# Optimization experiments

Hardware: AMD Instinct MI355X
Metric: run time of the kernel (lower is better)

The kernel has to match this reference:

```python
import jax, jax.numpy as jnp
import numpy as np

K = 16            # neighbors
RATIO = 0.25      # sampling ratio
BN_EPS = 1e-5


def setup_inputs() -> dict:
    key = jax.random.key(0)
    k1, k2, k3 = jax.random.split(key, 3)
    B, N, Cin, Cout = 8, 8192, 64, 128
    x = jax.random.normal(k1, (B, N, Cin), dtype=jnp.float32)
    p1 = jax.random.uniform(k2, (B, N, 3), dtype=jnp.float32)
    W = jax.random.normal(k3, (Cout, Cin), dtype=jnp.float32) * 0.05  # Conv1d(k=1, bias=False)
    gamma = jnp.ones((Cout,), dtype=jnp.float32)   # BatchNorm1d weight
    beta = jnp.zeros((Cout,), dtype=jnp.float32)   # BatchNorm1d bias
    return {"x": x, "p1": p1, "W": W, "gamma": gamma, "beta": beta}


def furthest_point_sample(p, M):
    """Greedy FPS. p: (B,N,3) -> (B,M) int32 indices. Starts at index 0 (CUDA impl convention)."""
    B, N, _ = p.shape
    first = jnp.zeros((B,), dtype=jnp.int32)
    mind = jnp.full((B, N), 1e10, dtype=p.dtype)

    def step(carry, _):
        mind, last = carry
        lp = jnp.take_along_axis(p, last[:, None, None].astype(jnp.int32), axis=1)  # (B,1,3)
        d = jnp.sum((p - lp) ** 2, axis=-1)          # (B,N)
        mind = jnp.minimum(mind, d)
        nxt = jnp.argmax(mind, axis=1).astype(jnp.int32)
        return (mind, nxt), nxt

    (_, _), rest = jax.lax.scan(step, (mind, first), None, length=M - 1)  # rest: (M-1,B)
    idx = jnp.concatenate([first[None, :], rest], axis=0)  # (M,B)
    return idx.T  # (B,M)


def reference(x, p1, W, gamma, beta):
    B, N, Cin = x.shape
    M = int(N * RATIO)

    # --- FPS sampling + gather coords ---
    fps_idx = furthest_point_sample(p1, M)                      # (B,M)
    p2 = jnp.take_along_axis(p1, fps_idx[:, :, None], axis=1)   # (B,M,3)

    # --- brute-force kNN of p1 around each p2 query ---
    d2 = (jnp.sum(p2 ** 2, -1)[:, :, None]
          - 2.0 * jnp.einsum('bmd,bnd->bmn', p2, p1)
          + jnp.sum(p1 ** 2, -1)[:, None, :])                   # (B,M,N)
    _, nbr = jax.lax.top_k(-d2, K)                              # (B,M,K) indices into N

    # --- shared MLP: 1x1 conv (no bias) + BatchNorm1d (training-mode stats) + ReLU ---
    h = jnp.einsum('bnc,oc->bno', x, W)                         # (B,N,Cout)
    mean = jnp.mean(h, axis=(0, 1))
    var = jnp.var(h, axis=(0, 1))
    h = (h - mean) * jax.lax.rsqrt(var + BN_EPS) * gamma + beta
    h = jax.nn.relu(h)

    # --- gather k neighbors per sampled point, max-pool over neighborhood ---
    feats = h[jnp.arange(B)[:, None, None], nbr]                # (B,M,K,Cout)
    y = jnp.max(feats, axis=2)                                  # (B,M,Cout)
    return y, p2
```

## Files before the change

### kernel.cpp

```cpp
#include <hip/hip_runtime.h>
#include <stdint.h>

#define Bb   8
#define Nn   8192
#define CIN  64
#define COUT 128
#define Mm   2048
#define KNN  16
#define NTOT (Bb*Nn)

typedef unsigned long long ull;


__device__ __forceinline__ float wave_max16(float x)
{
    int v = __float_as_int(x), t;
    t = __builtin_amdgcn_update_dpp(v, v, 0x111, 0xf, 0xf, false);
    v = __float_as_int(fmaxf(__int_as_float(v), __int_as_float(t)));
    t = __builtin_amdgcn_update_dpp(v, v, 0x112, 0xf, 0xf, false);
    v = __float_as_int(fmaxf(__int_as_float(v), __int_as_float(t)));
    t = __builtin_amdgcn_update_dpp(v, v, 0x114, 0xf, 0xf, false);
    v = __float_as_int(fmaxf(__int_as_float(v), __int_as_float(t)));
    t = __builtin_amdgcn_update_dpp(v, v, 0x118, 0xf, 0xf, false);
    v = __float_as_int(fmaxf(__int_as_float(v), __int_as_float(t)));
    unsigned r0 = (unsigned)__builtin_amdgcn_readlane(v, 15);
    unsigned r1 = (unsigned)__builtin_amdgcn_readlane(v, 31);
    unsigned r2 = (unsigned)__builtin_amdgcn_readlane(v, 47);
    unsigned r3 = (unsigned)__builtin_amdgcn_readlane(v, 63);
    unsigned m0 = r0 > r1 ? r0 : r1;
    unsigned m1 = r2 > r3 ? r2 : r3;
    unsigned mm = m0 > m1 ? m0 : m1;
    return __uint_as_float(mm);
}

__global__ __launch_bounds__(512, 1)
void fps_kernel(const float* __restrict__ p1, float* __restrict__ p2out)
{
    __shared__ float px[Nn], py[Nn], pz[Nn];
    __shared__ ull   wkey[2][8];
    const int b    = blockIdx.x;
    const int tid  = threadIdx.x;
    const int lane = tid & 63, wid = tid >> 6;
    const float* pb = p1 + b * Nn * 3;

    for (int i = tid; i < Nn * 3; i += 512) {
        float v = pb[i];
        int pt = i / 3;
        int c  = i - pt * 3;
        if (c == 0) px[pt] = v; else if (c == 1) py[pt] = v; else pz[pt] = v;
    }
    __syncthreads();

    float ppx[16], ppy[16], ppz[16], mind[16];
#pragma unroll
    for (int i = 0; i < 16; ++i) {
        int j = tid * 16 + i;
        ppx[i] = px[j]; ppy[i] = py[j]; ppz[i] = pz[j];
        mind[i] = 1e10f;
    }

    float lx = px[0], ly = py[0], lz = pz[0];
    if (tid == 0) {
        int o = (b * Mm) * 3;
        p2out[o] = lx; p2out[o + 1] = ly; p2out[o + 2] = lz;
    }

    for (int m = 1; m < Mm; ++m) {
        const int buf = m & 1;
        float bestv = -1.0f; int bestj = 0;
#pragma unroll
        for (int i = 0; i < 16; ++i) {
            float dx = __fsub_rn(ppx[i], lx);
            float dy = __fsub_rn(ppy[i], ly);
            float dz = __fsub_rn(ppz[i], lz);
            float d  = __fadd_rn(__fadd_rn(__fmul_rn(dx, dx), __fmul_rn(dy, dy)),
                                 __fmul_rn(dz, dz));
            float mv = fminf(mind[i], d);
            mind[i] = mv;
            if (mv > bestv) { bestv = mv; bestj = tid * 16 + i; }
        }

        float wv = wave_max16(bestv);
        ull tie = __ballot(bestv == wv);
        int low = __ffsll((long long)tie) - 1;
        if (lane == low) {
            wkey[buf][wid] = ((ull)__float_as_uint(wv) << 32) |
                             (unsigned int)(~(unsigned int)bestj);
        }
        __syncthreads();

        ull fk = wkey[buf][0];
#pragma unroll
        for (int w = 1; w < 8; ++w) { ull k = wkey[buf][w]; fk = k > fk ? k : fk; }
        int jw = (int)(~(unsigned int)fk);
        lx = px[jw]; ly = py[jw]; lz = pz[jw];
        if (tid == 0) {
            int o = (b * Mm + m) * 3;
            p2out[o] = lx; p2out[o + 1] = ly; p2out[o + 2] = lz;
        }
    }
}

__device__ __forceinline__ ull d2key(
    float qx, float qy, float qz, float qn, float x, float y, float z, int j)
{
    float dot = __fadd_rn(__fadd_rn(__fmul_rn(qx, x), __fmul_rn(qy, y)),
                          __fmul_rn(qz, z));
    float cn  = __fadd_rn(__fadd_rn(__fmul_rn(x, x), __fmul_rn(y, y)),
                          __fmul_rn(z, z));
    float d2  = __fadd_rn(__fsub_rn(qn, __fadd_rn(dot, dot)), cn);
    unsigned int bits = __float_as_uint(d2);
    unsigned int u = bits ^ (((unsigned int)((int)bits >> 31)) | 0x80000000u);
    return ((ull)u << 32) | (unsigned int)j;
}

__global__ __launch_bounds__(1024, 1)
void topk_kernel(const float* __restrict__ p1, const float* __restrict__ p2o,
                 int* __restrict__ nbr)
{
    __shared__ float px[Nn], py[Nn], pz[Nn];
    const int tid   = threadIdx.x;
    const int b     = blockIdx.x >> 7;
    const int mbase = (blockIdx.x & 127) << 4;
    const float* pb = p1 + b * Nn * 3;

    for (int i = tid; i < Nn * 3; i += 1024) {
        float v = pb[i];
        int pt = i / 3;
        int c  = i - pt * 3;
        if (c == 0) px[pt] = v; else if (c == 1) py[pt] = v; else pz[pt] = v;
    }
    __syncthreads();

    const int wid = tid >> 6, lane = tid & 63;
    const int qrow = b * Mm + mbase + wid;
    float qx = p2o[qrow * 3], qy = p2o[qrow * 3 + 1], qz = p2o[qrow * 3 + 2];
    float qn = __fadd_rn(__fadd_rn(__fmul_rn(qx, qx), __fmul_rn(qy, qy)),
                         __fmul_rn(qz, qz));

    const ull INV = ~0ull;
    ull k1 = INV, k2 = INV, k3 = INV;
#pragma unroll 4
    for (int i = 0; i < 128; ++i) {
        int j = lane + (i << 6);
        ull key = d2key(qx, qy, qz, qn, px[j], py[j], pz[j], j);
        bool b1 = key < k1, b2 = key < k2, b3 = key < k3;
        ull n1 = b1 ? key : k1;
        ull n2 = b1 ? k1 : (b2 ? key : k2);
        ull n3 = b2 ? k2 : (b3 ? key : k3);
        k1 = n1; k2 = n2; k3 = n3;
    }

    int* out = nbr + qrow * KNN;
    for (int r = 0; r < KNN; ++r) {
        ull wk = k1;
#pragma unroll
        for (int off = 1; off < 64; off <<= 1) {
            ull ok = __shfl_xor(wk, off, 64);
            wk = ok < wk ? ok : wk;
        }
        if (lane == 0) out[r] = (int)(unsigned int)(wk & 0xFFFFFFFFull);
        if (k1 == wk) { k1 = k2; k2 = k3; k3 = INV; }
        if (k1 == INV) {
            for (int i = 0; i < 128; ++i) {
                int j = lane + (i << 6);
                ull key = d2key(qx, qy, qz, qn, px[j], py[j], pz[j], j);
                if (key > wk) {
                    bool b1 = key < k1, b2 = key < k2, b3 = key < k3;
                    ull n1 = b1 ? key : k1;
                    ull n2 = b1 ? k1 : (b2 ? key : k2);
                    ull n3 = b2 ? k2 : (b3 ? key : k3);
                    k1 = n1; k2 = n2; k3 = n3;
                }
            }
        }
    }
}

__global__ __launch_bounds__(256)
void gemm_kernel(const float* __restrict__ x, const float* __restrict__ W,
                 float* __restrict__ h)
{
    const int r0 = blockIdx.x * 16 + (threadIdx.x >> 6) * 4;
    const int cp = threadIdx.x & 63;
    const float4* xp = (const float4*)(x + r0 * CIN);
    const float4* w0 = (const float4*)(W + (cp * 2) * CIN);
    const float4* w1 = (const float4*)(W + (cp * 2 + 1) * CIN);
    float a[4][2];
#pragma unroll
    for (int r = 0; r < 4; ++r) { a[r][0] = 0.f; a[r][1] = 0.f; }
#pragma unroll
    for (int k = 0; k < CIN / 4; ++k) {
        float4 wa = w0[k], wb = w1[k];
#pragma unroll
        for (int r = 0; r < 4; ++r) {
            float4 xv = xp[r * 16 + k];
            a[r][0] = fmaf(xv.x, wa.x, fmaf(xv.y, wa.y, fmaf(xv.z, wa.z, fmaf(xv.w, wa.w, a[r][0]))));
            a[r][1] = fmaf(xv.x, wb.x, fmaf(xv.y, wb.y, fmaf(xv.z, wb.z, fmaf(xv.w, wb.w, a[r][1]))));
        }
    }
#pragma unroll
    for (int r = 0; r < 4; ++r)
        *(float2*)(h + (r0 + r) * COUT + cp * 2) = make_float2(a[r][0], a[r][1]);
}

__global__ __launch_bounds__(256)
void stats_kernel(const float* __restrict__ h, float* __restrict__ stats)
{
    __shared__ float4 rs[256], rq[256];
    const int tid  = threadIdx.x;
    const int c4   = (tid & 31) * 4;
    const int rsub = tid >> 5;
    const int rbase = blockIdx.x * 256;
    float4 s = make_float4(0, 0, 0, 0), q = make_float4(0, 0, 0, 0);
    for (int i = 0; i < 32; ++i) {
        int r = rbase + rsub + i * 8;
        float4 v = *(const float4*)(h + r * COUT + c4);
        s.x += v.x; s.y += v.y; s.z += v.z; s.w += v.w;
        q.x = fmaf(v.x, v.x, q.x); q.y = fmaf(v.y, v.y, q.y);
        q.z = fmaf(v.z, v.z, q.z); q.w = fmaf(v.w, v.w, q.w);
    }
    rs[tid] = s; rq[tid] = q;
    __syncthreads();
    if (tid < 32) {
        for (int j = 1; j < 8; ++j) {
            float4 o = rs[tid + 32 * j];
            s.x += o.x; s.y += o.y; s.z += o.z; s.w += o.w;
            float4 oq = rq[tid + 32 * j];
            q.x += oq.x; q.y += oq.y; q.z += oq.z; q.w += oq.w;
        }
        atomicAdd(&stats[c4 + 0], s.x); atomicAdd(&stats[c4 + 1], s.y);
        atomicAdd(&stats[c4 + 2], s.z); atomicAdd(&stats[c4 + 3], s.w);
        atomicAdd(&stats[128 + c4 + 0], q.x); atomicAdd(&stats[128 + c4 + 1], q.y);
        atomicAdd(&stats[128 + c4 + 2], q.z); atomicAdd(&stats[128 + c4 + 3], q.w);
    }
}

__global__ void finalize_kernel(const float* __restrict__ stats,
                                const float* __restrict__ gamma,
                                const float* __restrict__ beta,
                                float* __restrict__ sb)
{
    int c = threadIdx.x;
    float mean = stats[c] * (1.0f / 65536.0f);
    float var  = stats[128 + c] * (1.0f / 65536.0f) - mean * mean;
    float scale = gamma[c] / sqrtf(var + 1e-5f);
    float bias  = beta[c] - mean * scale;
    sb[c] = scale; sb[128 + c] = bias;
}

__global__ __launch_bounds__(256)
void gather_kernel(const float* __restrict__ h, const int* __restrict__ nbr,
                   const float* __restrict__ sb, float* __restrict__ y)
{
    const int wid = threadIdx.x >> 6, lane = threadIdx.x & 63;
    const int t4 = blockIdx.x * 4 + wid;
    const int b  = t4 >> 11;
    const int c0 = lane * 2;
    float s0 = sb[c0], s1 = sb[c0 + 1];
    float b0 = sb[128 + c0], b1 = sb[128 + c0 + 1];
    const int* nb = nbr + t4 * KNN;
    float a0 = -1e30f, a1 = -1e30f;
#pragma unroll
    for (int k = 0; k < KNN; ++k) {
        int idx = nb[k];
        float2 v = *(const float2*)(h + ((b << 13) + idx) * COUT + c0);
        a0 = fmaxf(a0, fmaf(v.x, s0, b0));
        a1 = fmaxf(a1, fmaf(v.y, s1, b1));
    }
    a0 = fmaxf(a0, 0.0f); a1 = fmaxf(a1, 0.0f);
    *(float2*)(y + t4 * COUT + c0) = make_float2(a0, a1);
}

extern "C" void kernel_launch(void* const* d_in, const int* in_sizes, int n_in,
                              void* d_out, int out_size, void* d_ws, size_t ws_size,
                              hipStream_t stream)
{
    const float* x     = (const float*)d_in[0];
    const float* p1    = (const float*)d_in[1];
    const float* W     = (const float*)d_in[2];
    const float* gamma = (const float*)d_in[3];
    const float* beta  = (const float*)d_in[4];

    float* y  = (float*)d_out;
    float* p2 = (float*)d_out + Bb * Mm * COUT;

    char*  ws    = (char*)d_ws;
    float* h     = (float*)ws;
    int*   nbr   = (int*)(ws + 33619968);
    float* stats = (float*)(ws + 35717120);
    float* sb    = (float*)(ws + 35718144);

    hipMemsetAsync(stats, 0, 1024, stream);
    fps_kernel<<<Bb, 512, 0, stream>>>(p1, p2);
    gemm_kernel<<<NTOT / 16, 256, 0, stream>>>(x, W, h);
    stats_kernel<<<256, 256, 0, stream>>>(h, stats);
    finalize_kernel<<<1, 128, 0, stream>>>(stats, gamma, beta, sb);
    topk_kernel<<<Bb * 128, 1024, 0, stream>>>(p1, p2, nbr);
    gather_kernel<<<Bb * Mm / 4, 256, 0, stream>>>(h, nbr, sb, y);
}
```

Baseline: 2.329 ms.

## Halve FPS block to 4 waves and use packed FP32 math for 32 points/thread

The furthest-point-sampling kernel now runs 256 threads per batch instead of 512, and each thread owns 32 points held as float2 pairs. Distance math uses v_pk_add_f32/v_pk_mul_f32, and two candidate maxima are tracked per thread before the wave reduction. The cross-wave reduction shrinks from 8 to 4 keys. The aim is to cut the per-iteration barrier and reduction cost in this latency-bound serial loop, at the cost of more per-thread work and register pressure. Subtracting via adding the negation should stay bit-exact, and tie-breaking keeps the lowest index.

```diff
diff --git a/kernel.cpp b/kernel.cpp
--- a/kernel.cpp
+++ b/kernel.cpp
@@ -10,7 +10,13 @@
 #define NTOT (Bb*Nn)
 
 typedef unsigned long long ull;
-
+typedef float v2f __attribute__((ext_vector_type(2)));
+
+
+__device__ __forceinline__ v2f pk_add(v2f a, v2f b)
+{ v2f d; asm("v_pk_add_f32 %0, %1, %2" : "=v"(d) : "v"(a), "v"(b)); return d; }
+__device__ __forceinline__ v2f pk_mul(v2f a, v2f b)
+{ v2f d; asm("v_pk_mul_f32 %0, %1, %2" : "=v"(d) : "v"(a), "v"(b)); return d; }
 
 __device__ __forceinline__ float wave_max16(float x)
 {
@@ -33,17 +39,17 @@
     return __uint_as_float(mm);
 }
 
-__global__ __launch_bounds__(512, 1)
+__global__ __launch_bounds__(256, 1)
 void fps_kernel(const float* __restrict__ p1, float* __restrict__ p2out)
 {
     __shared__ float px[Nn], py[Nn], pz[Nn];
-    __shared__ ull   wkey[2][8];
+    __shared__ alignas(16) ull wkey[2][4];
     const int b    = blockIdx.x;
     const int tid  = threadIdx.x;
     const int lane = tid & 63, wid = tid >> 6;
     const float* pb = p1 + b * Nn * 3;
 
-    for (int i = tid; i < Nn * 3; i += 512) {
+    for (int i = tid; i < Nn * 3; i += 256) {
         float v = pb[i];
         int pt = i / 3;
         int c  = i - pt * 3;
@@ -51,12 +57,14 @@
     }
     __syncthreads();
 
-    float ppx[16], ppy[16], ppz[16], mind[16];
+    v2f ppx[16], ppy[16], ppz[16], mind[16];
 #pragma unroll
     for (int i = 0; i < 16; ++i) {
-        int j = tid * 16 + i;
-        ppx[i] = px[j]; ppy[i] = py[j]; ppz[i] = pz[j];
-        mind[i] = 1e10f;
+        int j0 = tid * 32 + 2 * i;
+        ppx[i] = (v2f){px[j0], px[j0 + 1]};
+        ppy[i] = (v2f){py[j0], py[j0 + 1]};
+        ppz[i] = (v2f){pz[j0], pz[j0 + 1]};
+        mind[i] = (v2f){1e10f, 1e10f};
     }
 
     float lx = px[0], ly = py[0], lz = pz[0];
@@ -67,18 +75,26 @@
 
     for (int m = 1; m < Mm; ++m) {
         const int buf = m & 1;
-        float bestv = -1.0f; int bestj = 0;
+        float nx = -lx, ny = -ly, nz = -lz;
+        v2f nx2 = (v2f){nx, nx}, ny2 = (v2f){ny, ny}, nz2 = (v2f){nz, nz};
+        float bv0 = -1.0f, bv1 = -1.0f; int bj0 = 0, bj1 = 1;
 #pragma unroll
         for (int i = 0; i < 16; ++i) {
-            float dx = __fsub_rn(ppx[i], lx);
-            float dy = __fsub_rn(ppy[i], ly);
-            float dz = __fsub_rn(ppz[i], lz);
-            float d  = __fadd_rn(__fadd_rn(__fmul_rn(dx, dx), __fmul_rn(dy, dy)),
-                                 __fmul_rn(dz, dz));
-            float mv = fminf(mind[i], d);
-            mind[i] = mv;
-            if (mv > bestv) { bestv = mv; bestj = tid * 16 + i; }
-        }
+            v2f dx = pk_add(ppx[i], nx2);
+            v2f dy = pk_add(ppy[i], ny2);
+            v2f dz = pk_add(ppz[i], nz2);
+            v2f s  = pk_add(pk_add(pk_mul(dx, dx), pk_mul(dy, dy)),
+                            pk_mul(dz, dz));
+            float m0 = fminf(mind[i].x, s.x);
+            float m1 = fminf(mind[i].y, s.y);
+            mind[i].x = m0; mind[i].y = m1;
+            if (m0 > bv0) { bv0 = m0; bj0 = 2 * i; }
+            if (m1 > bv1) { bv1 = m1; bj1 = 2 * i + 1; }
+        }
+        float bestv; int bestj;
+        if (bv1 > bv0 || (bv1 == bv0 && bj1 < bj0)) { bestv = bv1; bestj = bj1; }
+        else                                        { bestv = bv0; bestj = bj0; }
+        bestj += tid * 32;
 
         float wv = wave_max16(bestv);
         ull tie = __ballot(bestv == wv);
@@ -89,9 +105,11 @@
         }
         __syncthreads();
 
-        ull fk = wkey[buf][0];
-#pragma unroll
-        for (int w = 1; w < 8; ++w) { ull k = wkey[buf][w]; fk = k > fk ? k : fk; }
+        ull k0 = wkey[buf][0], k1 = wkey[buf][1];
+        ull k2 = wkey[buf][2], k3 = wkey[buf][3];
+        ull k01 = k0 > k1 ? k0 : k1;
+        ull k23 = k2 > k3 ? k2 : k3;
+        ull fk  = k01 > k23 ? k01 : k23;
         int jw = (int)(~(unsigned int)fk);
         lx = px[jw]; ly = py[jw]; lz = pz[jw];
         if (tid == 0) {
@@ -292,7 +310,7 @@
     float* sb    = (float*)(ws + 35718144);
 
     hipMemsetAsync(stats, 0, 1024, stream);
-    fps_kernel<<<Bb, 512, 0, stream>>>(p1, p2);
+    fps_kernel<<<Bb, 256, 0, stream>>>(p1, p2);
     gemm_kernel<<<NTOT / 16, 256, 0, stream>>>(x, W, h);
     stats_kernel<<<256, 256, 0, stream>>>(h, stats);
     finalize_kernel<<<1, 128, 0, stream>>>(stats, gamma, beta, sb);
```

After: 2.293 ms. No clear change (-1.5%).
